# Performance work log

Hardware: AMD Instinct MI355X
Metric: run time of the kernel (lower is better)

The kernel has to match this reference:

```python
import jax, jax.numpy as jnp
import numpy as np

B, C, H, W = 32, 3, 512, 512
OUT = (64, 64)  # (out_grid[0]=Nx, out_grid[1]=Ny)
SMALL = 1e-4


def setup_inputs() -> dict:
    key = jax.random.key(0)
    k1, k2 = jax.random.split(key, 2)
    X = jax.random.normal(k1, (B, C, H, W), dtype=jnp.float32)
    fan_in = C * H * W
    # localization net: flatten + dense(5); scaled so p ~ N(0,1) and exp(p) is stable
    W_loc = jax.random.normal(k2, (fan_in, 5), dtype=jnp.float32) / np.float32(np.sqrt(fan_in))
    b_loc = jnp.zeros((5,), dtype=jnp.float32)
    return {"X": X, "W_loc": W_loc, "b_loc": b_loc}


def reference(X, W_loc, b_loc):
    Bn = X.shape[0]
    # locnet: p = flatten(X) @ W_loc + b_loc  -> [B, 5]
    p = X.reshape(Bn, -1) @ W_loc + b_loc

    N = min(OUT)
    gx = OUT[0] * (p[:, 0] + 1.0) / 2.0          # [B]
    gy = OUT[1] * (p[:, 1] + 1.0) / 2.0          # [B]
    sigma2 = jnp.exp(p[:, 2])                    # [B]
    delta = jnp.exp(p[:, 3]) * (max(W, H) - 1) / (N - 1.0)  # [B]
    gamma = jnp.exp(p[:, 4])                     # [B]

    i1 = jnp.arange(OUT[0], dtype=jnp.float32)   # [Nx]
    i2 = jnp.arange(OUT[1], dtype=jnp.float32)   # [Ny]
    a = jnp.arange(W, dtype=jnp.float32)         # [W]
    b = jnp.arange(H, dtype=jnp.float32)         # [H]

    mx = gx[:, None] + delta[:, None] * (i1 - N / 2.0 - 0.5)  # [B, Nx]
    my = gy[:, None] + delta[:, None] * (i2 - N / 2.0 - 0.5)  # [B, Ny]

    Fx = jnp.exp(-((a - mx[:, :, None]) ** 2) / (2.0 * sigma2[:, None, None]))  # [B,Nx,W]
    Fx = Fx / (Fx.sum(axis=-1, keepdims=True) + SMALL)
    Fy = jnp.exp(-((b - my[:, :, None]) ** 2) / (2.0 * sigma2[:, None, None]))  # [B,Ny,H]
    Fy = Fy / (Fy.sum(axis=-1, keepdims=True) + SMALL)

    # glimpse read: gamma * Fy @ X @ Fx^T, done as batched contractions
    Fyx = jnp.einsum('bnh,bchw->bcnw', Fy, X)        # [B,C,Ny,W]
    out = jnp.einsum('bcnw,bmw->bcnm', Fyx, Fx)      # [B,C,Ny,Nx]
    return gamma[:, None, None, None] * out
```

## Files before the change

kernel.cpp:

```cpp
#include <hip/hip_runtime.h>
#include <math.h>

#define B_ 32
#define C_ 3
#define H_ 512
#define W_ 512
#define NOUT 64
#define FAN (C_*H_*W_)

#define CHUNKS 384
#define CELEMS (FAN / CHUNKS)
#define NB 16
#define BGROUPS (B_ / NB)

#define FXH_OFF 1024
#define ARR_ELEMS (B_*NOUT*W_)

typedef __bf16 bf16x8 __attribute__((ext_vector_type(8)));
typedef float f32x4 __attribute__((ext_vector_type(4)));

__device__ __forceinline__ unsigned short f2bf(float f) {
    unsigned int u = __float_as_uint(f);
    u = (u + 0x7FFFu + ((u >> 16) & 1u)) >> 16;
    return (unsigned short)u;
}
__device__ __forceinline__ float bf2f(unsigned short h) {
    return __uint_as_float(((unsigned int)h) << 16);
}
__device__ __forceinline__ void cvt_hilo(const float* x, bf16x8* hi, bf16x8* lo) {
    union { unsigned int u[4]; bf16x8 v; } H, L;
    #pragma unroll
    for (int i = 0; i < 4; i++) {
        unsigned short h0 = f2bf(x[2*i]),  h1 = f2bf(x[2*i+1]);
        H.u[i] = (unsigned int)h0 | ((unsigned int)h1 << 16);
        unsigned short l0 = f2bf(x[2*i]   - bf2f(h0));
        unsigned short l1 = f2bf(x[2*i+1] - bf2f(h1));
        L.u[i] = (unsigned int)l0 | ((unsigned int)l1 << 16);
    }
    *hi = H.v; *lo = L.v;
}

__global__ __launch_bounds__(256, 3) void k_locnet(const float* __restrict__ X,
                                                   const float* __restrict__ Wl,
                                                   float* __restrict__ ws) {
    const int chunk = blockIdx.x;
    const int b0 = blockIdx.y * NB;
    const int t = threadIdx.x;

    float acc[NB][5] = {};
    const size_t base = (size_t)chunk * CELEMS;

    for (int k = t; k < CELEMS / 4; k += 256) {
        const size_t i0 = base + (size_t)k * 4;
        const float4* W4 = (const float4*)(Wl + i0 * 5);
        float4 w0 = W4[0], w1 = W4[1], w2 = W4[2], w3 = W4[3], w4 = W4[4];
        float wv[20] = {w0.x, w0.y, w0.z, w0.w,
                        w1.x, w1.y, w1.z, w1.w,
                        w2.x, w2.y, w2.z, w2.w,
                        w3.x, w3.y, w3.z, w3.w,
                        w4.x, w4.y, w4.z, w4.w};
        #pragma unroll
        for (int bb = 0; bb < NB; bb++) {
            float4 x = *(const float4*)(X + (size_t)(b0 + bb) * FAN + i0);
            float xv[4] = {x.x, x.y, x.z, x.w};
            #pragma unroll
            for (int e = 0; e < 4; e++)
                #pragma unroll
                for (int j = 0; j < 5; j++)
                    acc[bb][j] += xv[e] * wv[e * 5 + j];
        }
    }

    #pragma unroll
    for (int off = 32; off > 0; off >>= 1)
        #pragma unroll
        for (int bb = 0; bb < NB; bb++)
            #pragma unroll
            for (int j = 0; j < 5; j++)
                acc[bb][j] += __shfl_down(acc[bb][j], off);

    __shared__ float sred[4][NB * 5];
    const int wave = t >> 6, lane = t & 63;
    if (lane == 0) {
        #pragma unroll
        for (int bb = 0; bb < NB; bb++)
            #pragma unroll
            for (int j = 0; j < 5; j++)
                sred[wave][bb * 5 + j] = acc[bb][j];
    }
    __syncthreads();
    if (t < NB * 5) {
        float s = sred[0][t] + sred[1][t] + sred[2][t] + sred[3][t];
        atomicAdd(&ws[b0 * 5 + t], s);
    }
}

__global__ __launch_bounds__(256) void k_filters(const float* __restrict__ bl,
                                                 void* __restrict__ wsv) {
    const int n = blockIdx.x;
    const int b = blockIdx.y;
    const int which = blockIdx.z;
    const int t = threadIdx.x;

    const float* pw = (const float*)wsv;
    unsigned short* arrh = (unsigned short*)((char*)wsv + FXH_OFF) + (size_t)which * 2 * ARR_ELEMS;
    unsigned short* arrl = arrh + ARR_ELEMS;

    const float p0 = pw[b * 5 + 0] + bl[0];
    const float p1 = pw[b * 5 + 1] + bl[1];
    const float p2 = pw[b * 5 + 2] + bl[2];
    const float p3 = pw[b * 5 + 3] + bl[3];

    const float g = (which == 0) ? 32.f * (p0 + 1.f) : 32.f * (p1 + 1.f);
    const float inv2s = 0.5f / expf(p2);
    const float delta = expf(p3) * (511.0f / 63.0f);
    const float mean = g + delta * ((float)n - 32.5f);

    float d0 = (float)t - mean;
    float f0 = expf(-d0 * d0 * inv2s);
    float d1 = (float)(t + 256) - mean;
    float f1 = expf(-d1 * d1 * inv2s);

    float s = f0 + f1;
    #pragma unroll
    for (int off = 32; off > 0; off >>= 1) s += __shfl_down(s, off);
    __shared__ float sred[4];
    __shared__ float stot;
    const int wave = t >> 6, lane = t & 63;
    if (lane == 0) sred[wave] = s;
    __syncthreads();
    if (t == 0) stot = sred[0] + sred[1] + sred[2] + sred[3] + 1e-4f;
    __syncthreads();
    const float scale = 1.0f / stot;

    const size_t o = ((size_t)b * NOUT + n) * W_;
    float v0 = f0 * scale, v1 = f1 * scale;
    unsigned short h0 = f2bf(v0), h1 = f2bf(v1);
    arrh[o + t] = h0;
    arrh[o + t + 256] = h1;
    arrl[o + t] = f2bf(v0 - bf2f(h0));
    arrl[o + t + 256] = f2bf(v1 - bf2f(h1));
}

#define GP 72

__global__ __launch_bounds__(256) void k_glimpse(const float* __restrict__ X,
                                                 const float* __restrict__ bl,
                                                 const void* __restrict__ wsv,
                                                 float* __restrict__ out) {
    const int hc = blockIdx.x;
    const int bc = blockIdx.y;
    const int b = bc / 3;
    const int t = threadIdx.x;
    const int lane = t & 63;
    const int wv = t >> 6;
    const int l15 = lane & 15;
    const int quad = lane >> 4;
    const int hbase = hc * 64;

    const float* pw = (const float*)wsv;
    const unsigned short* fxh = (const unsigned short*)((const char*)wsv + FXH_OFF) + (size_t)b * NOUT * W_;
    const unsigned short* fxl = fxh + ARR_ELEMS;
    const unsigned short* fyh = fxh + 2 * ARR_ELEMS;
    const unsigned short* fyl = fxh + 3 * ARR_ELEMS;

    __shared__ __align__(16) unsigned short Gh[64 * GP];
    __shared__ __align__(16) unsigned short Gl[64 * GP];

    const float* Xp = X + (size_t)bc * (H_ * W_);

    f32x4 ahh[4] = {}, axl[4] = {};
    const size_t arow = (size_t)(hbase + 16 * wv + l15) * W_;
    #pragma unroll 4
    for (int ks = 0; ks < 16; ks++) {
        const int ko = ks * 32 + quad * 8;
        float xa[8];
        *(float4*)&xa[0] = *(const float4*)(Xp + arow + ko);
        *(float4*)&xa[4] = *(const float4*)(Xp + arow + ko + 4);
        bf16x8 ah, al;
        cvt_hilo(xa, &ah, &al);
        #pragma unroll
        for (int mt = 0; mt < 4; mt++) {
            const int fo = (16 * mt + l15) * W_ + ko;
            bf16x8 bh  = *(const bf16x8*)&fxh[fo];
            bf16x8 bl2 = *(const bf16x8*)&fxl[fo];
            ahh[mt] = __builtin_amdgcn_mfma_f32_16x16x32_bf16(ah, bh,  ahh[mt], 0, 0, 0);
            axl[mt] = __builtin_amdgcn_mfma_f32_16x16x32_bf16(al, bh,  axl[mt], 0, 0, 0);
            axl[mt] = __builtin_amdgcn_mfma_f32_16x16x32_bf16(ah, bl2, axl[mt], 0, 0, 0);
        }
    }

    #pragma unroll
    for (int mt = 0; mt < 4; mt++) {
        unsigned short gh[4], gl[4];
        #pragma unroll
        for (int r = 0; r < 4; r++) {
            float g = ahh[mt][r] + axl[mt][r];
            gh[r] = f2bf(g);
            gl[r] = f2bf(g - bf2f(gh[r]));
        }
        int o = (16 * mt + l15) * GP + 16 * wv + quad * 4;
        *(uint2*)&Gh[o] = make_uint2((unsigned int)gh[0] | ((unsigned int)gh[1] << 16),
                                     (unsigned int)gh[2] | ((unsigned int)gh[3] << 16));
        *(uint2*)&Gl[o] = make_uint2((unsigned int)gl[0] | ((unsigned int)gl[1] << 16),
                                     (unsigned int)gl[2] | ((unsigned int)gl[3] << 16));
    }
    __syncthreads();

    f32x4 ph[4] = {}, px[4] = {};
    const size_t yrow = (size_t)(16 * wv + l15) * W_ + hbase;
    #pragma unroll
    for (int ks = 0; ks < 2; ks++) {
        const int ko = ks * 32 + quad * 8;
        bf16x8 yh = *(const bf16x8*)&fyh[yrow + ko];
        bf16x8 yl = *(const bf16x8*)&fyl[yrow + ko];
        #pragma unroll
        for (int mt = 0; mt < 4; mt++) {
            const int go = (16 * mt + l15) * GP + ko;
            bf16x8 gh = *(const bf16x8*)&Gh[go];
            bf16x8 gl = *(const bf16x8*)&Gl[go];
            ph[mt] = __builtin_amdgcn_mfma_f32_16x16x32_bf16(yh, gh, ph[mt], 0, 0, 0);
            px[mt] = __builtin_amdgcn_mfma_f32_16x16x32_bf16(yl, gh, px[mt], 0, 0, 0);
            px[mt] = __builtin_amdgcn_mfma_f32_16x16x32_bf16(yh, gl, px[mt], 0, 0, 0);
        }
    }

    const float gamma = expf(pw[b * 5 + 4] + bl[4]);
    float* outp = out + (size_t)bc * (NOUT * NOUT);
    #pragma unroll
    for (int mt = 0; mt < 4; mt++)
        #pragma unroll
        for (int r = 0; r < 4; r++) {
            int n = 16 * wv + quad * 4 + r;
            int m = 16 * mt + l15;
            atomicAdd(&outp[n * NOUT + m], gamma * (ph[mt][r] + px[mt][r]));
        }
}

extern "C" void kernel_launch(void* const* d_in, const int* in_sizes, int n_in,
                              void* d_out, int out_size, void* d_ws, size_t ws_size,
                              hipStream_t stream) {
    const float* X  = (const float*)d_in[0];
    const float* Wl = (const float*)d_in[1];
    const float* bl = (const float*)d_in[2];
    float* out = (float*)d_out;
    float* ws  = (float*)d_ws;

    hipMemsetAsync(ws, 0, 1024, stream);
    hipMemsetAsync(out, 0, (size_t)out_size * sizeof(float), stream);

    k_locnet<<<dim3(CHUNKS, BGROUPS), 256, 0, stream>>>(X, Wl, ws);
    k_filters<<<dim3(NOUT, B_, 2), 256, 0, stream>>>(bl, d_ws);
    k_glimpse<<<dim3(8, B_ * C_), 256, 0, stream>>>(X, bl, d_ws, out);
}
```

Baseline: 248.8 us.

## Restructure locnet GEMV to stage weights in LDS and cover all batches per block

The locnet reduction is rewritten so each block stages a 1024-element chunk of W_loc (times 5 outputs) into shared memory once. Eight threads handle each of the 32 batches and read X with strided float4 loads. Partial sums are reduced with an 8-lane xor shuffle, then atomically added per batch. This replaces the 16-batch register tiling, which needed 80 accumulators per thread, loaded W twice across batch groups, and ran a full wave reduction. The new scheme costs more atomics (768 blocks × 32 batches × 5) and reads weights from LDS with strided access that may cause bank conflicts.

```diff
diff --git a/kernel.cpp b/kernel.cpp
--- a/kernel.cpp
+++ b/kernel.cpp
@@ -8,10 +8,8 @@
 #define NOUT 64
 #define FAN (C_*H_*W_)
 
-#define CHUNKS 384
-#define CELEMS (FAN / CHUNKS)
-#define NB 16
-#define BGROUPS (B_ / NB)
+#define LCHUNKS 768
+#define LCE 1024
 
 #define FXH_OFF 1024
 #define ARR_ELEMS (B_*NOUT*W_)
@@ -40,58 +38,50 @@
     *hi = H.v; *lo = L.v;
 }
 
-__global__ __launch_bounds__(256, 3) void k_locnet(const float* __restrict__ X,
-                                                   const float* __restrict__ Wl,
-                                                   float* __restrict__ ws) {
+__global__ __launch_bounds__(256) void k_locnet(const float* __restrict__ X,
+                                                const float* __restrict__ Wl,
+                                                float* __restrict__ ws) {
     const int chunk = blockIdx.x;
-    const int b0 = blockIdx.y * NB;
     const int t = threadIdx.x;
-
-    float acc[NB][5] = {};
-    const size_t base = (size_t)chunk * CELEMS;
-
-    for (int k = t; k < CELEMS / 4; k += 256) {
-        const size_t i0 = base + (size_t)k * 4;
-        const float4* W4 = (const float4*)(Wl + i0 * 5);
-        float4 w0 = W4[0], w1 = W4[1], w2 = W4[2], w3 = W4[3], w4 = W4[4];
-        float wv[20] = {w0.x, w0.y, w0.z, w0.w,
-                        w1.x, w1.y, w1.z, w1.w,
-                        w2.x, w2.y, w2.z, w2.w,
-                        w3.x, w3.y, w3.z, w3.w,
-                        w4.x, w4.y, w4.z, w4.w};
-        #pragma unroll
-        for (int bb = 0; bb < NB; bb++) {
-            float4 x = *(const float4*)(X + (size_t)(b0 + bb) * FAN + i0);
-            float xv[4] = {x.x, x.y, x.z, x.w};
+    const size_t kbase = (size_t)chunk * LCE;
+
+    __shared__ __align__(16) float Wlds[LCE * 5];
+    {
+        const float4* Wg = (const float4*)(Wl + kbase * 5);
+        #pragma unroll
+        for (int i = 0; i < 5; i++)
+            *(float4*)&Wlds[(t + 256 * i) * 4] = Wg[t + 256 * i];
+    }
+    __syncthreads();
+
+    const int bb = t >> 3;
+    const int j8 = t & 7;
+    const float* Xr = X + (size_t)bb * FAN + kbase;
+
+    float acc[5] = {};
+    #pragma unroll 8
+    for (int i = 0; i < 32; i++) {
+        const int k0 = (j8 + 8 * i) * 4;
+        float4 x = *(const float4*)(Xr + k0);
+        const float* wr = &Wlds[k0 * 5];
+        float xa[4] = {x.x, x.y, x.z, x.w};
+        #pragma unroll
+        for (int e = 0; e < 4; e++)
             #pragma unroll
-            for (int e = 0; e < 4; e++)
-                #pragma unroll
-                for (int j = 0; j < 5; j++)
-                    acc[bb][j] += xv[e] * wv[e * 5 + j];
-        }
-    }
-
-    #pragma unroll
-    for (int off = 32; off > 0; off >>= 1)
-        #pragma unroll
-        for (int bb = 0; bb < NB; bb++)
-            #pragma unroll
-            for (int j = 0; j < 5; j++)
-                acc[bb][j] += __shfl_down(acc[bb][j], off);
-
-    __shared__ float sred[4][NB * 5];
-    const int wave = t >> 6, lane = t & 63;
-    if (lane == 0) {
-        #pragma unroll
-        for (int bb = 0; bb < NB; bb++)
-            #pragma unroll
-            for (int j = 0; j < 5; j++)
-                sred[wave][bb * 5 + j] = acc[bb][j];
-    }
-    __syncthreads();
-    if (t < NB * 5) {
-        float s = sred[0][t] + sred[1][t] + sred[2][t] + sred[3][t];
-        atomicAdd(&ws[b0 * 5 + t], s);
+            for (int jj = 0; jj < 5; jj++)
+                acc[jj] += xa[e] * wr[e * 5 + jj];
+    }
+
+    #pragma unroll
+    for (int off = 1; off < 8; off <<= 1)
+        #pragma unroll
+        for (int jj = 0; jj < 5; jj++)
+            acc[jj] += __shfl_xor(acc[jj], off);
+
+    if (j8 == 0) {
+        #pragma unroll
+        for (int jj = 0; jj < 5; jj++)
+            atomicAdd(&ws[bb * 5 + jj], acc[jj]);
     }
 }
 
@@ -249,7 +239,7 @@
     hipMemsetAsync(ws, 0, 1024, stream);
     hipMemsetAsync(out, 0, (size_t)out_size * sizeof(float), stream);
 
-    k_locnet<<<dim3(CHUNKS, BGROUPS), 256, 0, stream>>>(X, Wl, ws);
+    k_locnet<<<dim3(LCHUNKS), 256, 0, stream>>>(X, Wl, ws);
     k_filters<<<dim3(NOUT, B_, 2), 256, 0, stream>>>(bl, d_ws);
     k_glimpse<<<dim3(8, B_ * C_), 256, 0, stream>>>(X, bl, d_ws, out);
 }
```

Result: slower. 349.7 us (+40.6%).
